# Kernel optimization log

Measured on AMD Instinct MI355X. Metric: run time of the kernel, lower is better.

## Reference

```python
import jax, jax.numpy as jnp
import numpy as np

GRID_W, GRID_H = 4, 4          # num_splits = (4, 4) -> 16 experts
N = 524288                     # number of sample points
IN_DIM, HID, OUT = 2, 256, 3   # per-expert MLP: 2 -> 256 -> 3


def setup_inputs() -> dict:
    key = jax.random.key(0)
    k_s, k_w1, k_w2 = jax.random.split(key, 3)
    E = GRID_W * GRID_H
    samples = jax.random.uniform(k_s, (N, IN_DIM), dtype=jnp.float32)
    W1 = jax.random.normal(k_w1, (E, IN_DIM, HID), dtype=jnp.float32) * (1.0 / np.sqrt(IN_DIM))
    b1 = jnp.zeros((E, HID), dtype=jnp.float32)
    W2 = jax.random.normal(k_w2, (E, HID, OUT), dtype=jnp.float32) * (1.0 / np.sqrt(HID))
    b2 = jnp.zeros((E, OUT), dtype=jnp.float32)
    return {"samples": samples, "W1": W1, "b1": b1, "W2": W2, "b2": b2}


def _grid_inds(samples):
    # i, j = floor(samples[:, d] * n).clip(0, n-1); inds = j * w + i
    i = jnp.clip(jnp.floor(samples[:, 0] * GRID_W), 0, GRID_W - 1)
    j = jnp.clip(jnp.floor(samples[:, 1] * GRID_H), 0, GRID_H - 1)
    return (j * GRID_W + i).astype(jnp.int32)  # [N]


def reference(samples, W1, b1, W2, b2):
    inds = _grid_inds(samples)                     # [N] expert id per sample
    E = W1.shape[0]
    out = jnp.zeros((samples.shape[0], W2.shape[-1]), dtype=samples.dtype)
    # Dense dispatch: loop over the small fixed set of experts (16) and
    # select each sample's own expert output via the routing mask. Same
    # math as torch's features[inds == i] gather + scatter combine.
    for e in range(E):
        h = jax.nn.relu(samples @ W1[e] + b1[e])   # [N, HID]
        y = h @ W2[e] + b2[e]                      # [N, OUT]
        out = jnp.where((inds == e)[:, None], y, out)
    return out
```

## Files before the change

### kernel.cpp

```cpp
#include <hip/hip_runtime.h>

typedef _Float16 h2 __attribute__((ext_vector_type(2)));

#define GRID_W 4
#define GRID_H 4
#define NEXP   16
#define HID    256
#define TPB    512
#define S      2
#define SAMP   (TPB * S)
#define NWAVE  (TPB / 64)
#define GR     64
#define MAXENT 33

#define CAPP   88
#define HPA    (2 * CAPP)
#define HPE    (6 * HPA)
#define F4PA   (CAPP / 4)
#define F4PE   (6 * F4PA)

#define OFFB_AFF  33792
#define OFFB_SLOT 34560
#define OFFB_I    43264
#define NSLOT     (SAMP + GR)
#define LDS_BYTES (OFFB_I + 4 * (16 + 17 + 17 + 3 * MAXENT + 1 + NEXP))

union H8 { float4 f; h2 p[4]; };

__global__ __launch_bounds__(TPB, 6) void fused_moe_kernel(
    const float2* __restrict__ samples,
    const float*  __restrict__ W1, const float* __restrict__ b1,
    const float*  __restrict__ W2, const float* __restrict__ b2,
    float* __restrict__ out, int N)
{
    extern __shared__ __align__(16) char smem[];
    _Float16* sMix = (_Float16*)smem;
    float*    sAff = (float*)(smem + OFFB_AFF);
    int2*     sSlot= (int2*)(smem + OFFB_SLOT);
    int*      sI   = (int*)(smem + OFFB_I);
    int* sHist = sI;
    int* sOff  = sI + 16;
    int* sES   = sI + 33;
    int* sEexp = sI + 50;
    int* sEbas = sI + 50 + MAXENT;
    int* sEcnt = sI + 50 + 2 * MAXENT;
    int* sC    = sI + 50 + 3 * MAXENT;
    int* sM2   = sI + 51 + 3 * MAXENT;

    const int tid = threadIdx.x;
    const int lane = tid & 63, wv = tid >> 6;
    if (tid < NEXP) sHist[tid] = 0;
    __syncthreads();

    const int base0 = blockIdx.x * SAMP;
    float px[S], py[S]; int eid[S], rank[S], gid[S]; bool act[S];
#pragma unroll
    for (int s = 0; s < S; ++s) {
        gid[s] = base0 + s * TPB + tid;
        act[s] = gid[s] < N;
        float2 p = act[s] ? samples[gid[s]] : make_float2(0.f, 0.f);
        px[s] = p.x; py[s] = p.y;
        int i = (int)(p.x * (float)GRID_W); i = i < 0 ? 0 : (i > GRID_W - 1 ? GRID_W - 1 : i);
        int j = (int)(p.y * (float)GRID_H); j = j < 0 ? 0 : (j > GRID_H - 1 ? GRID_H - 1 : j);
        eid[s] = j * GRID_W + i;
        rank[s] = act[s] ? atomicAdd(&sHist[eid[s]], 1) : 0;
    }

#pragma unroll
    for (int ee = 0; ee < 2; ++ee) {
        int e = 2 * wv + ee;
        float aff[9] = {0.f,0.f,0.f,0.f,0.f,0.f,0.f,0.f,0.f};
        int basep = 0;
        _Float16* mb = sMix + e * HPE;
        int ci = e & 3, cj = e >> 2;
        float x0 = ci * 0.25f, x1 = x0 + 0.25f;
        float y0c = cj * 0.25f, y1c = y0c + 0.25f;
#pragma unroll
        for (int kc = 0; kc < 4; ++kc) {
            int k = kc * 64 + lane;
            float a  = W1[e * 512 + k];
            float b  = W1[e * 512 + 256 + k];
            float c  = b1[e * 256 + k];
            float u0 = W2[e * 768 + 3 * k];
            float u1 = W2[e * 768 + 3 * k + 1];
            float u2 = W2[e * 768 + 3 * k + 2];
            float vmin = fminf(a * x0, a * x1) + fminf(b * y0c, b * y1c) + c;
            float vmax = fmaxf(a * x0, a * x1) + fmaxf(b * y0c, b * y1c) + c;
            bool on = vmin >= 0.f;
            bool mixed = (!on) && (vmax > 0.f);
            if (on) {
                aff[0] += u0 * a; aff[1] += u0 * b; aff[2] += u0 * c;
                aff[3] += u1 * a; aff[4] += u1 * b; aff[5] += u1 * c;
                aff[6] += u2 * a; aff[7] += u2 * b; aff[8] += u2 * c;
            }
            unsigned long long mk = __ballot(mixed);
            int pos = basep + __popcll(mk & ((1ull << lane) - 1ull));
            if (mixed && pos < HPA) {
                mb[pos]           = (_Float16)a;
                mb[HPA + pos]     = (_Float16)b;
                mb[2 * HPA + pos] = (_Float16)c;
                mb[3 * HPA + pos] = (_Float16)u0;
                mb[4 * HPA + pos] = (_Float16)u1;
                mb[5 * HPA + pos] = (_Float16)u2;
            }
            basep += __popcll(mk);
        }
        if (basep > HPA) basep = HPA;
        int padTo = (basep + 7) & ~7;
        int idx = basep + lane;
        if (idx < padTo) {
            _Float16 z = (_Float16)0.f;
            mb[idx] = z; mb[HPA + idx] = z; mb[2 * HPA + idx] = z;
            mb[3 * HPA + idx] = z; mb[4 * HPA + idx] = z; mb[5 * HPA + idx] = z;
        }
#pragma unroll
        for (int j = 0; j < 9; ++j) {
            float v = aff[j];
            for (int d = 1; d < 64; d <<= 1) v += __shfl_xor(v, d);
            aff[j] = v;
        }
        if (lane == 0) {
            float* af = sAff + e * 12;
            af[0] = aff[0]; af[1] = aff[1]; af[2] = aff[2] + b2[3 * e];
            af[3] = aff[3]; af[4] = aff[4]; af[5] = aff[5] + b2[3 * e + 1];
            af[6] = aff[6]; af[7] = aff[7]; af[8] = aff[8] + b2[3 * e + 2];
            af[9] = 0.f; af[10] = 0.f; af[11] = 0.f;
            sM2[e] = padTo >> 3;
        }
    }
    __syncthreads();

    if (tid == 0) {
        int acc = 0, ec = 0;
        for (int e = 0; e < NEXP; ++e) {
            sOff[e] = acc; acc += sHist[e];
            sES[e] = ec;  ec  += (sHist[e] + GR - 1) >> 6;
        }
        sOff[NEXP] = acc; sES[NEXP] = ec; *sC = ec;
    }
    __syncthreads();

#pragma unroll
    for (int s = 0; s < S; ++s) {
        if (act[s]) {
            union { h2 h; int i; } u;
            u.h.x = (_Float16)px[s]; u.h.y = (_Float16)py[s];
            int2 v; v.x = u.i; v.y = gid[s];
            sSlot[sOff[eid[s]] + rank[s]] = v;
        }
    }
    int C = *sC;
    if (tid < C) {
        int e = 0;
        while (tid >= sES[e + 1]) ++e;
        int j = tid - sES[e];
        sEexp[tid] = e;
        sEbas[tid] = sOff[e] + j * GR;
        sEcnt[tid] = min(GR, sHist[e] - j * GR);
    }
    __syncthreads();

    for (int c = wv; c < C; c += NWAVE) {
        int e   = __builtin_amdgcn_readfirstlane(sEexp[c]);
        int bas = __builtin_amdgcn_readfirstlane(sEbas[c]);
        int cnt = __builtin_amdgcn_readfirstlane(sEcnt[c]);

        int2 v = sSlot[bas + lane];
        union { int i; h2 h; } uxy; uxy.i = v.x;
        float x = (float)uxy.h.x, y = (float)uxy.h.y;
        int qg = v.y;

        const float* af = sAff + e * 12;
        float y0 = fmaf(x, af[0], fmaf(y, af[1], af[2]));
        float y1 = fmaf(x, af[3], fmaf(y, af[4], af[5]));
        float y2 = fmaf(x, af[6], fmaf(y, af[7], af[8]));

        h2 px2; px2.x = uxy.h.x; px2.y = uxy.h.x;
        h2 py2; py2.x = uxy.h.y; py2.y = uxy.h.y;

        int nb = __builtin_amdgcn_readfirstlane(sM2[e]);
        const float4* Wm = (const float4*)sMix + e * F4PE;
        for (int bi = 0; bi < nb; ++bi) {
            H8 A, B, Cc, U0, U1, U2;
            A.f  = Wm[bi];
            B.f  = Wm[F4PA + bi];
            Cc.f = Wm[2 * F4PA + bi];
            U0.f = Wm[3 * F4PA + bi];
            U1.f = Wm[4 * F4PA + bi];
            U2.f = Wm[5 * F4PA + bi];
#pragma unroll
            for (int j = 0; j < 4; ++j) {
                h2 h = __builtin_elementwise_fma(px2, A.p[j],
                       __builtin_elementwise_fma(py2, B.p[j], Cc.p[j]));
                h2 z = (h2)(_Float16)0.0f;
                h = __builtin_elementwise_max(h, z);
#if __has_builtin(__builtin_amdgcn_fdot2)
                y0 = __builtin_amdgcn_fdot2(h, U0.p[j], y0, false);
                y1 = __builtin_amdgcn_fdot2(h, U1.p[j], y1, false);
                y2 = __builtin_amdgcn_fdot2(h, U2.p[j], y2, false);
#else
                y0 += (float)h.x * (float)U0.p[j].x + (float)h.y * (float)U0.p[j].y;
                y1 += (float)h.x * (float)U1.p[j].x + (float)h.y * (float)U1.p[j].y;
                y2 += (float)h.x * (float)U2.p[j].x + (float)h.y * (float)U2.p[j].y;
#endif
            }
        }

        if (lane < cnt) {
            int d = 3 * qg;
            out[d + 0] = y0; out[d + 1] = y1; out[d + 2] = y2;
        }
    }
}

extern "C" void kernel_launch(void* const* d_in, const int* in_sizes, int n_in,
                              void* d_out, int out_size, void* d_ws, size_t ws_size,
                              hipStream_t stream) {
    const float* samples = (const float*)d_in[0];
    const float* W1      = (const float*)d_in[1];
    const float* b1      = (const float*)d_in[2];
    const float* W2      = (const float*)d_in[3];
    const float* b2      = (const float*)d_in[4];
    float* out = (float*)d_out;

    const int N = in_sizes[0] / 2;
    const int nblocks = (N + SAMP - 1) / SAMP;

    fused_moe_kernel<<<nblocks, TPB, LDS_BYTES, stream>>>(
        (const float2*)samples, W1, b1, W2, b2, out, N);
}
```

Baseline: 79.27 us.

## Hoist per-expert weight preprocessing into a separate prep kernel via workspace

Moves the per-expert classification of hidden units (always-on folded into an affine map, mixed units packed to fp16) out of every block into a one-time 16-block prep kernel that writes to the workspace. The main kernel then reads the affine coefficients and mixed weights from global memory instead of LDS, which shrinks LDS use and raises launch_bounds occupancy to 8. The serial single-thread prefix sum is replaced by a wave-level shuffle scan. This adds a second launch, and the inner loop now does global/L2 loads where it previously read LDS.

Result: faster. 77.51 us (median of 2 runs) (-2.2%).

```diff
diff --git a/kernel.cpp b/kernel.cpp
--- a/kernel.cpp
+++ b/kernel.cpp
@@ -19,25 +19,90 @@
 #define F4PA   (CAPP / 4)
 #define F4PE   (6 * F4PA)
 
-#define OFFB_AFF  33792
-#define OFFB_SLOT 34560
-#define OFFB_I    43264
-#define NSLOT     (SAMP + GR)
-#define LDS_BYTES (OFFB_I + 4 * (16 + 17 + 17 + 3 * MAXENT + 1 + NEXP))
+#define WSOFF_M2  768
+#define WSOFF_MIX 1024
+
+#define NSLOT  (SAMP + GR)
+#define OFFB_I (NSLOT * 8)
+#define LDS_BYTES (OFFB_I + 4 * (16 + 17 + 17 + 3 * MAXENT + 1))
 
 union H8 { float4 f; h2 p[4]; };
 
-__global__ __launch_bounds__(TPB, 6) void fused_moe_kernel(
+__global__ __launch_bounds__(64) void prep_kernel(
+    const float* __restrict__ W1, const float* __restrict__ b1,
+    const float* __restrict__ W2, const float* __restrict__ b2,
+    float* __restrict__ wsAff, int* __restrict__ wsM2,
+    _Float16* __restrict__ wsMix) {
+    const int e = blockIdx.x, lane = threadIdx.x;
+    float aff[9] = {0.f,0.f,0.f,0.f,0.f,0.f,0.f,0.f,0.f};
+    int basep = 0;
+    _Float16* mb = wsMix + e * HPE;
+    int ci = e & 3, cj = e >> 2;
+    float x0 = ci * 0.25f, x1 = x0 + 0.25f;
+    float y0c = cj * 0.25f, y1c = y0c + 0.25f;
+#pragma unroll
+    for (int kc = 0; kc < 4; ++kc) {
+        int k = kc * 64 + lane;
+        float a  = W1[e * 512 + k];
+        float b  = W1[e * 512 + 256 + k];
+        float c  = b1[e * 256 + k];
+        float u0 = W2[e * 768 + 3 * k];
+        float u1 = W2[e * 768 + 3 * k + 1];
+        float u2 = W2[e * 768 + 3 * k + 2];
+        float vmin = fminf(a * x0, a * x1) + fminf(b * y0c, b * y1c) + c;
+        float vmax = fmaxf(a * x0, a * x1) + fmaxf(b * y0c, b * y1c) + c;
+        bool on = vmin >= 0.f;
+        bool mixed = (!on) && (vmax > 0.f);
+        if (on) {
+            aff[0] += u0 * a; aff[1] += u0 * b; aff[2] += u0 * c;
+            aff[3] += u1 * a; aff[4] += u1 * b; aff[5] += u1 * c;
+            aff[6] += u2 * a; aff[7] += u2 * b; aff[8] += u2 * c;
+        }
+        unsigned long long mk = __ballot(mixed);
+        int pos = basep + __popcll(mk & ((1ull << lane) - 1ull));
+        if (mixed && pos < HPA) {
+            mb[pos]           = (_Float16)a;
+            mb[HPA + pos]     = (_Float16)b;
+            mb[2 * HPA + pos] = (_Float16)c;
+            mb[3 * HPA + pos] = (_Float16)u0;
+            mb[4 * HPA + pos] = (_Float16)u1;
+            mb[5 * HPA + pos] = (_Float16)u2;
+        }
+        basep += __popcll(mk);
+    }
+    if (basep > HPA) basep = HPA;
+    int padTo = (basep + 7) & ~7;
+    int idx = basep + lane;
+    if (idx < padTo) {
+        _Float16 z = (_Float16)0.f;
+        mb[idx] = z; mb[HPA + idx] = z; mb[2 * HPA + idx] = z;
+        mb[3 * HPA + idx] = z; mb[4 * HPA + idx] = z; mb[5 * HPA + idx] = z;
+    }
+#pragma unroll
+    for (int j = 0; j < 9; ++j) {
+        float v = aff[j];
+        for (int d = 1; d < 64; d <<= 1) v += __shfl_xor(v, d);
+        aff[j] = v;
+    }
+    if (lane == 0) {
+        float* af = wsAff + e * 12;
+        af[0] = aff[0]; af[1] = aff[1]; af[2] = aff[2] + b2[3 * e];
+        af[3] = aff[3]; af[4] = aff[4]; af[5] = aff[5] + b2[3 * e + 1];
+        af[6] = aff[6]; af[7] = aff[7]; af[8] = aff[8] + b2[3 * e + 2];
+        af[9] = 0.f; af[10] = 0.f; af[11] = 0.f;
+        wsM2[e] = padTo >> 3;
+    }
+}
+
+__global__ __launch_bounds__(TPB, 8) void fused_moe_kernel(
     const float2* __restrict__ samples,
-    const float*  __restrict__ W1, const float* __restrict__ b1,
-    const float*  __restrict__ W2, const float* __restrict__ b2,
+    const float* __restrict__ wsAff, const int* __restrict__ wsM2,
+    const _Float16* __restrict__ wsMix,
     float* __restrict__ out, int N)
 {
     extern __shared__ __align__(16) char smem[];
-    _Float16* sMix = (_Float16*)smem;
-    float*    sAff = (float*)(smem + OFFB_AFF);
-    int2*     sSlot= (int2*)(smem + OFFB_SLOT);
-    int*      sI   = (int*)(smem + OFFB_I);
+    int2* sSlot = (int2*)smem;
+    int*  sI    = (int*)(smem + OFFB_I);
     int* sHist = sI;
     int* sOff  = sI + 16;
     int* sES   = sI + 33;
@@ -45,7 +110,6 @@
     int* sEbas = sI + 50 + MAXENT;
     int* sEcnt = sI + 50 + 2 * MAXENT;
     int* sC    = sI + 50 + 3 * MAXENT;
-    int* sM2   = sI + 51 + 3 * MAXENT;
 
     const int tid = threadIdx.x;
     const int lane = tid & 63, wv = tid >> 6;
@@ -65,78 +129,19 @@
         eid[s] = j * GRID_W + i;
         rank[s] = act[s] ? atomicAdd(&sHist[eid[s]], 1) : 0;
     }
-
-#pragma unroll
-    for (int ee = 0; ee < 2; ++ee) {
-        int e = 2 * wv + ee;
-        float aff[9] = {0.f,0.f,0.f,0.f,0.f,0.f,0.f,0.f,0.f};
-        int basep = 0;
-        _Float16* mb = sMix + e * HPE;
-        int ci = e & 3, cj = e >> 2;
-        float x0 = ci * 0.25f, x1 = x0 + 0.25f;
-        float y0c = cj * 0.25f, y1c = y0c + 0.25f;
-#pragma unroll
-        for (int kc = 0; kc < 4; ++kc) {
-            int k = kc * 64 + lane;
-            float a  = W1[e * 512 + k];
-            float b  = W1[e * 512 + 256 + k];
-            float c  = b1[e * 256 + k];
-            float u0 = W2[e * 768 + 3 * k];
-            float u1 = W2[e * 768 + 3 * k + 1];
-            float u2 = W2[e * 768 + 3 * k + 2];
-            float vmin = fminf(a * x0, a * x1) + fminf(b * y0c, b * y1c) + c;
-            float vmax = fmaxf(a * x0, a * x1) + fmaxf(b * y0c, b * y1c) + c;
-            bool on = vmin >= 0.f;
-            bool mixed = (!on) && (vmax > 0.f);
-            if (on) {
-                aff[0] += u0 * a; aff[1] += u0 * b; aff[2] += u0 * c;
-                aff[3] += u1 * a; aff[4] += u1 * b; aff[5] += u1 * c;
-                aff[6] += u2 * a; aff[7] += u2 * b; aff[8] += u2 * c;
-            }
-            unsigned long long mk = __ballot(mixed);
-            int pos = basep + __popcll(mk & ((1ull << lane) - 1ull));
-            if (mixed && pos < HPA) {
-                mb[pos]           = (_Float16)a;
-                mb[HPA + pos]     = (_Float16)b;
-                mb[2 * HPA + pos] = (_Float16)c;
-                mb[3 * HPA + pos] = (_Float16)u0;
-                mb[4 * HPA + pos] = (_Float16)u1;
-                mb[5 * HPA + pos] = (_Float16)u2;
-            }
-            basep += __popcll(mk);
-        }
-        if (basep > HPA) basep = HPA;
-        int padTo = (basep + 7) & ~7;
-        int idx = basep + lane;
-        if (idx < padTo) {
-            _Float16 z = (_Float16)0.f;
-            mb[idx] = z; mb[HPA + idx] = z; mb[2 * HPA + idx] = z;
-            mb[3 * HPA + idx] = z; mb[4 * HPA + idx] = z; mb[5 * HPA + idx] = z;
-        }
-#pragma unroll
-        for (int j = 0; j < 9; ++j) {
-            float v = aff[j];
-            for (int d = 1; d < 64; d <<= 1) v += __shfl_xor(v, d);
-            aff[j] = v;
-        }
-        if (lane == 0) {
-            float* af = sAff + e * 12;
-            af[0] = aff[0]; af[1] = aff[1]; af[2] = aff[2] + b2[3 * e];
-            af[3] = aff[3]; af[4] = aff[4]; af[5] = aff[5] + b2[3 * e + 1];
-            af[6] = aff[6]; af[7] = aff[7]; af[8] = aff[8] + b2[3 * e + 2];
-            af[9] = 0.f; af[10] = 0.f; af[11] = 0.f;
-            sM2[e] = padTo >> 3;
-        }
-    }
-    __syncthreads();
-
-    if (tid == 0) {
-        int acc = 0, ec = 0;
-        for (int e = 0; e < NEXP; ++e) {
-            sOff[e] = acc; acc += sHist[e];
-            sES[e] = ec;  ec  += (sHist[e] + GR - 1) >> 6;
-        }
-        sOff[NEXP] = acc; sES[NEXP] = ec; *sC = ec;
+    __syncthreads();
+
+    if (wv == 0) {
+        int h  = (lane < NEXP) ? sHist[lane] : 0;
+        int ec = (lane < NEXP) ? ((h + 63) >> 6) : 0;
+        int sh = h, se = ec;
+#pragma unroll
+        for (int d = 1; d < 16; d <<= 1) {
+            int th = __shfl_up(sh, d), te = __shfl_up(se, d);
+            if (lane >= d) { sh += th; se += te; }
+        }
+        if (lane < NEXP) { sOff[lane] = sh - h; sES[lane] = se - ec; }
+        if (lane == NEXP - 1) { sOff[NEXP] = sh; sES[NEXP] = se; *sC = se; }
     }
     __syncthreads();
 
@@ -170,7 +175,7 @@
         float x = (float)uxy.h.x, y = (float)uxy.h.y;
         int qg = v.y;
 
-        const float* af = sAff + e * 12;
+        const float* af = wsAff + e * 12;
         float y0 = fmaf(x, af[0], fmaf(y, af[1], af[2]));
         float y1 = fmaf(x, af[3], fmaf(y, af[4], af[5]));
         float y2 = fmaf(x, af[6], fmaf(y, af[7], af[8]));
@@ -178,8 +183,8 @@
         h2 px2; px2.x = uxy.h.x; px2.y = uxy.h.x;
         h2 py2; py2.x = uxy.h.y; py2.y = uxy.h.y;
 
-        int nb = __builtin_amdgcn_readfirstlane(sM2[e]);
-        const float4* Wm = (const float4*)sMix + e * F4PE;
+        int nb = __builtin_amdgcn_readfirstlane(wsM2[e]);
+        const float4* Wm = (const float4*)wsMix + e * F4PE;
         for (int bi = 0; bi < nb; ++bi) {
             H8 A, B, Cc, U0, U1, U2;
             A.f  = Wm[bi];
@@ -224,8 +229,13 @@
     float* out = (float*)d_out;
 
     const int N = in_sizes[0] / 2;
+    float*    wsAff = (float*)d_ws;
+    int*      wsM2  = (int*)((char*)d_ws + WSOFF_M2);
+    _Float16* wsMix = (_Float16*)((char*)d_ws + WSOFF_MIX);
+
+    prep_kernel<<<NEXP, 64, 0, stream>>>(W1, b1, W2, b2, wsAff, wsM2, wsMix);
+
     const int nblocks = (N + SAMP - 1) / SAMP;
-
     fused_moe_kernel<<<nblocks, TPB, LDS_BYTES, stream>>>(
-        (const float2*)samples, W1, b1, W2, b2, out, N);
+        (const float2*)samples, wsAff, wsM2, wsMix, out, N);
 }
```
